# Optimization experiments

Hardware: AMD Instinct MI355X
Metric: run time of the kernel (lower is better)

Reference implementation:

```python
import jax, jax.numpy as jnp
import numpy as np

P, B, D, H, O = 512, 8, 256, 75, 128  # passage_len, batch, input_size, attn hidden, GRU hidden


def setup_inputs() -> dict:
    key = jax.random.key(0)
    ks = jax.random.split(key, 10)

    def w(k, shape, fan_in):
        return jax.random.normal(k, shape, jnp.float32) * (1.0 / np.sqrt(fan_in))

    return {
        "v": jax.random.normal(ks[0], (P, B, D), jnp.float32),
        "Wvp1": w(ks[1], (H, D), D),          # nn.Linear(input_size, hidden, bias=False)
        "Wvp2": w(ks[2], (H, D), D),
        "vw": w(ks[3], (H,), H),               # nn.Linear(hidden, 1, bias=False)
        "Wg": w(ks[4], (2 * D, 2 * D), 2 * D),  # Gate linear, no bias
        "w_ih_f": w(ks[5], (3 * O, 2 * D), 2 * D),
        "w_hh_f": w(ks[6], (3 * O, O), O),
        "b_ih_f": jnp.zeros((3 * O,), jnp.float32),
        "b_hh_f": jnp.zeros((3 * O,), jnp.float32),
        "w_ih_b": w(ks[7], (3 * O, 2 * D), 2 * D),
        "w_hh_b": w(ks[8], (3 * O, O), O),
        "b_ih_b": jnp.zeros((3 * O,), jnp.float32),
        "b_hh_b": jnp.zeros((3 * O,), jnp.float32),
    }


def _gru(x, w_ih, w_hh, b_ih, b_hh):
    # x: (T, B, in) -> hidden states (T, B, O); PyTorch GRU gate order (r, z, n)
    hdim = w_hh.shape[1]
    xp = x @ w_ih.T + b_ih  # precompute input projections: (T, B, 3O)

    def step(h, xp_t):
        gh = h @ w_hh.T + b_hh
        i_r, i_z, i_n = jnp.split(xp_t, 3, axis=-1)
        h_r, h_z, h_n = jnp.split(gh, 3, axis=-1)
        r = jax.nn.sigmoid(i_r + h_r)
        z = jax.nn.sigmoid(i_z + h_z)
        n = jnp.tanh(i_n + r * h_n)
        h_new = (1.0 - z) * n + z * h
        return h_new, h_new

    h0 = jnp.zeros((x.shape[1], hdim), x.dtype)
    _, hs = jax.lax.scan(step, h0, xp)
    return hs


def reference(v, Wvp1, Wvp2, vw, Wg,
              w_ih_f, w_hh_f, b_ih_f, b_hh_f,
              w_ih_b, w_hh_b, b_ih_b, b_hh_b):
    # dropout is inference no-op (and in the torch code its result is discarded anyway)
    Wv1 = v @ Wvp1.T  # (P, B, H) -- broadcast over key axis (dim 1 after expand)
    Wv2 = v @ Wvp2.T  # (P, B, H) -- broadcast over query axis
    # s[i, j, b, h] = tanh(Wv2[i] + Wv1[j]); softmax over i (keys)
    s = jnp.tanh(Wv2[:, None] + Wv1[None, :])          # (P, P, B, H)
    scores = jnp.einsum('ijbh,h->ijb', s, vw)          # (P, P, B)
    a = jax.nn.softmax(scores, axis=0)
    c = jnp.einsum('ijb,ibd->jbd', a, v)               # attended context (P, B, D)
    g = jnp.concatenate([v, c], axis=2)                # (P, B, 2D)
    g = jax.nn.sigmoid(g @ Wg.T) * g                   # Gate
    hf = _gru(g, w_ih_f, w_hh_f, b_ih_f, b_hh_f)
    hb = _gru(g[::-1], w_ih_b, w_hh_b, b_ih_b, b_hh_b)[::-1]
    return jnp.concatenate([hf, hb], axis=2)           # (P, B, 2O)
```

## Files before the change

kernel.cpp:

```cpp
#include <hip/hip_runtime.h>

#define TP 512
#define TB 8
#define TD 256
#define TH 75
#define THP 80
#define TO 128

#define LOG2E2 2.8853900817779268f

typedef _Float16 half_t;
typedef _Float16 half2v __attribute__((ext_vector_type(2)));
typedef _Float16 half4v __attribute__((ext_vector_type(4)));
typedef _Float16 half8v __attribute__((ext_vector_type(8)));
typedef float    float4v __attribute__((ext_vector_type(4)));

__device__ __forceinline__ float fast_rcp(float x) { return __builtin_amdgcn_rcpf(x); }
__device__ __forceinline__ float ex2(float x) {
#if __has_builtin(__builtin_amdgcn_exp2f)
    return __builtin_amdgcn_exp2f(x);
#else
    float r; asm("v_exp_f32 %0, %1" : "=v"(r) : "v"(x)); return r;
#endif
}
__device__ __forceinline__ float fast_tanh(float x) {
    return 1.0f - 2.0f * fast_rcp(1.0f + __expf(2.0f * x));
}
__device__ __forceinline__ float fast_sigmoid(float x) {
    return fast_rcp(1.0f + __expf(-x));
}
__device__ __forceinline__ float fdot2h(half2v a, half2v b, float c) {
#if __has_builtin(__builtin_amdgcn_fdot2)
    return __builtin_amdgcn_fdot2(a, b, c, false);
#else
    return c + (float)a[0] * (float)b[0] + (float)a[1] * (float)b[1];
#endif
}
#define EXT2(v, j) __builtin_shufflevector((v), (v), 2*(j), 2*(j)+1)
__device__ __forceinline__ void dot3_h8(half8v wr, half8v wz, half8v wn, half8v h,
                                        float& ar, float& az, float& an) {
    half2v h0 = EXT2(h, 0), h1 = EXT2(h, 1), h2 = EXT2(h, 2), h3 = EXT2(h, 3);
    ar = fdot2h(EXT2(wr, 0), h0, ar);
    az = fdot2h(EXT2(wz, 0), h0, az);
    an = fdot2h(EXT2(wn, 0), h0, an);
    ar = fdot2h(EXT2(wr, 1), h1, ar);
    az = fdot2h(EXT2(wz, 1), h1, az);
    an = fdot2h(EXT2(wn, 1), h1, an);
    ar = fdot2h(EXT2(wr, 2), h2, ar);
    az = fdot2h(EXT2(wz, 2), h2, az);
    an = fdot2h(EXT2(wn, 2), h2, an);
    ar = fdot2h(EXT2(wr, 3), h3, ar);
    az = fdot2h(EXT2(wz, 3), h3, az);
    an = fdot2h(EXT2(wn, 3), h3, an);
}
__device__ __forceinline__ float pair_sum_dpp(float v) {
    int i1 = __builtin_amdgcn_update_dpp(0, __builtin_bit_cast(int, v), 0xB1, 0xF, 0xF, true);
    return v + __builtin_bit_cast(float, i1);
}

__global__ __launch_bounds__(256) void prep_kernel(
    const float* __restrict__ v,
    const float* __restrict__ Wvp1, const float* __restrict__ Wvp2,
    const float* __restrict__ Wg,   const float* __restrict__ wihf,
    const float* __restrict__ wihb, const float* __restrict__ bihf,
    const float* __restrict__ bihb, const float* __restrict__ whhf,
    const float* __restrict__ whhb,
    float* __restrict__ bihC,
    half_t* __restrict__ v16, half_t* __restrict__ g16,
    half_t* __restrict__ Wg16B, half_t* __restrict__ Wih16B,
    half_t* __restrict__ whh16, half_t* __restrict__ WT16B,
    half_t* __restrict__ vT16)
{
    __shared__ half_t lt[64 * 66];

    if (blockIdx.x >= 7203) {
        int vb = blockIdx.x - 7203;
        int t = threadIdx.x;
        int b  = vb >> 5;
        int pt = (vb >> 2) & 7;
        int dt = vb & 3;
        {
            int pl = t >> 2, dseg = (t & 3) * 16;
            const float4* src = (const float4*)(v + (((pt * 64 + pl) * 8 + b) << 8) + dt * 64 + dseg);
            float4 f0 = src[0], f1 = src[1], f2 = src[2], f3 = src[3];
            half_t hv[16] = {
                (half_t)f0.x,(half_t)f0.y,(half_t)f0.z,(half_t)f0.w,
                (half_t)f1.x,(half_t)f1.y,(half_t)f1.z,(half_t)f1.w,
                (half_t)f2.x,(half_t)f2.y,(half_t)f2.z,(half_t)f2.w,
                (half_t)f3.x,(half_t)f3.y,(half_t)f3.z,(half_t)f3.w };
#pragma unroll
            for (int u = 0; u < 16; ++u) lt[(dseg + u) * 66 + pl] = hv[u];
        }
        __syncthreads();
        {
            int dl = t >> 2, pseg = (t & 3) * 16;
            half8v h0 = *(const half8v*)(lt + dl * 66 + pseg);
            half8v h1 = *(const half8v*)(lt + dl * 66 + pseg + 8);
            half8v* dst = (half8v*)(vT16 + ((b * 256 + dt * 64 + dl) << 9) + pt * 64 + pseg);
            dst[0] = h0; dst[1] = h1;
        }
        return;
    }

    int idx = blockIdx.x * 256 + threadIdx.x;
    if (idx < 1048576) {
        half_t val = (half_t)v[idx];
        v16[idx] = val;
        int row = idx >> 8, d = idx & 255;
        g16[row * 512 + d] = val;
        return;
    }
    idx -= 1048576;
    if (idx < 768) { bihC[idx] = (idx < 384) ? bihf[idx] : bihb[idx - 384]; return; }
    idx -= 768;
    if (idx < 262144) {
        int j = idx & 7, lane = (idx >> 3) & 63, kt = (idx >> 9) & 15, nt = idx >> 13;
        int o = nt * 16 + (lane & 15);
        int k = kt * 32 + ((lane >> 4) << 3) + j;
        Wg16B[idx] = (half_t)Wg[o * 512 + k];
        return;
    }
    idx -= 262144;
    if (idx < 393216) {
        int j = idx & 7, lane = (idx >> 3) & 63, kt = (idx >> 9) & 15, nt = idx >> 13;
        int o = nt * 16 + (lane & 15);
        int k = kt * 32 + ((lane >> 4) << 3) + j;
        Wih16B[idx] = (half_t)((o < 384) ? wihf[o * 512 + k] : wihb[(o - 384) * 512 + k]);
        return;
    }
    idx -= 393216;
    if (idx < 98304) {
        int d = idx / 49152, i = idx - d * 49152;
        whh16[idx] = (half_t)(d ? whhb[i] : whhf[i]);
        return;
    }
    idx -= 98304;
    if (idx < 40960) {
        int j = idx & 7, lane = (idx >> 3) & 63, kt = (idx >> 9) & 7, nt = idx >> 12;
        int o = nt * 16 + (lane & 15);
        int k = kt * 32 + ((lane >> 4) << 3) + j;
        float vv = 0.0f;
        if (o < 75)       vv = Wvp1[o * 256 + k];
        else if (o < 150) vv = Wvp2[(o - 75) * 256 + k];
        WT16B[idx] = (half_t)vv;
    }
}

__global__ __launch_bounds__(128) void wv12_kernel(
    const half_t* __restrict__ v16, const half_t* __restrict__ WT16B,
    float* __restrict__ Wv1, float* __restrict__ Wv2T)
{
    int tid = threadIdx.x;
    int lane = tid & 63, w = tid >> 6;
    int l15 = lane & 15, quad = lane >> 4;
    int r0 = blockIdx.x * 16;

    float4v acc[5];
#pragma unroll
    for (int n5 = 0; n5 < 5; ++n5) acc[n5] = (float4v){0.f, 0.f, 0.f, 0.f};

#pragma unroll
    for (int kt = 0; kt < 8; ++kt) {
        half8v a = *(const half8v*)(v16 + (r0 + l15) * 256 + kt * 32 + quad * 8);
#pragma unroll
        for (int n5 = 0; n5 < 5; ++n5) {
            int nt = w * 5 + n5;
            half8v b = *(const half8v*)(WT16B + ((nt * 8 + kt) * 64 + lane) * 8);
            acc[n5] = __builtin_amdgcn_mfma_f32_16x16x32_f16(a, b, acc[n5], 0, 0, 0);
        }
    }
#pragma unroll
    for (int n5 = 0; n5 < 5; ++n5) {
        int col = (w * 5 + n5) * 16 + l15;
#pragma unroll
        for (int r = 0; r < 4; ++r) {
            int row = r0 + quad * 4 + r;
            int p = row >> 3, b = row & 7;
            int ob = (b * TP + p) * THP;
            float val2 = LOG2E2 * acc[n5][r];
            if (col < 75)       Wv1[ob + col] = val2;
            else if (col < 80)  { Wv1[ob + col] = 0.0f;
                                  Wv2T[(b * THP + col - 75) * TP + p] = val2; }
            else if (col < 150) Wv2T[(b * THP + col - 75) * TP + p] = val2;
            else if (col < 155) Wv2T[(b * THP + col - 75) * TP + p] = 0.0f;
        }
    }
}

__global__ __launch_bounds__(256) void score_kernel(
    const float* __restrict__ Wv1, const float* __restrict__ Wv2T,
    const float* __restrict__ vw, const half_t* __restrict__ vT16,
    half_t* __restrict__ g16)
{
    int tid = threadIdx.x;
    int b  = blockIdx.x >> 6;
    int j0 = (blockIdx.x & 63) * 8;
    __shared__ float wv1j[8 * THP];
    __shared__ float vws[THP];
    __shared__ float sc[8 * TP];
    __shared__ __align__(16) half_t aL[16 * 528];

    int lane = tid & 63, w = tid >> 6;
    int l15 = lane & 15, quad = lane >> 4;

    for (int e = tid; e < 8 * 528; e += 256) aL[8 * 528 + e] = (half_t)0.0f;

    if (tid < THP) vws[tid] = (tid < TH) ? vw[tid] : 0.0f;
    for (int e = tid; e < 8 * THP; e += 256) {
        int jj = e / THP, k = e - jj * THP;
        wv1j[e] = Wv1[(b * TP + j0 + jj) * THP + k];
    }
    __syncthreads();

    float Csum = 0.0f;
    {
        const float4* c4 = (const float4*)vws;
        for (int kk = 0; kk < 20; ++kk) { float4 c = c4[kk]; Csum += c.x + c.y + c.z + c.w; }
    }

    int i0 = tid, i1 = tid + 256;
    float acc0[8] = {0.f,0.f,0.f,0.f,0.f,0.f,0.f,0.f};
    float acc1[8] = {0.f,0.f,0.f,0.f,0.f,0.f,0.f,0.f};
    const float* wvt = Wv2T + b * THP * TP;
#pragma unroll
    for (int kt = 0; kt < 5; ++kt) {
        float r0v[16], r1v[16];
#pragma unroll
        for (int u = 0; u < 16; ++u) {
            const float* colp = wvt + (kt * 16 + u) * TP;
            r0v[u] = colp[i0];
            r1v[u] = colp[i1];
        }
        const float* cp = vws + kt * 16;
#pragma unroll
        for (int jj = 0; jj < 8; ++jj) {
            const float* w1 = wv1j + jj * THP + kt * 16;
            float s0 = 0.f, s1 = 0.f;
#pragma unroll
            for (int u = 0; u < 16; ++u) {
                float cu = cp[u], wu = w1[u];
                s0 += cu * fast_rcp(1.0f + ex2(r0v[u] + wu));
                s1 += cu * fast_rcp(1.0f + ex2(r1v[u] + wu));
            }
            acc0[jj] += s0; acc1[jj] += s1;
        }
    }
#pragma unroll
    for (int jj = 0; jj < 8; ++jj) {
        sc[jj * TP + i0] = Csum - 2.0f * acc0[jj];
        sc[jj * TP + i1] = Csum - 2.0f * acc1[jj];
    }
    __syncthreads();

#pragma unroll
    for (int ps = 0; ps < 2; ++ps) {
        int jj = (tid >> 6) + ps * 4, l = tid & 63;
        float m = -1e30f;
#pragma unroll
        for (int q = 0; q < 8; ++q) m = fmaxf(m, sc[jj * TP + l + q * 64]);
#pragma unroll
        for (int s = 32; s > 0; s >>= 1) m = fmaxf(m, __shfl_xor(m, s));
        float e[8];
        float sum = 0.0f;
#pragma unroll
        for (int q = 0; q < 8; ++q) { e[q] = __expf(sc[jj * TP + l + q * 64] - m); sum += e[q]; }
#pragma unroll
        for (int s = 32; s > 0; s >>= 1) sum += __shfl_xor(sum, s);
        float inv = fast_rcp(sum);
#pragma unroll
        for (int q = 0; q < 8; ++q) aL[jj * 528 + l + q * 64] = (half_t)(e[q] * inv);
    }
    __syncthreads();

    {
        const half_t* vbase = vT16 + ((b * 256) << 9);
        float4v acc[4];
#pragma unroll
        for (int nti = 0; nti < 4; ++nti) acc[nti] = (float4v){0.f, 0.f, 0.f, 0.f};

#pragma unroll 4
        for (int kt = 0; kt < 16; ++kt) {
            half8v a = *(const half8v*)(aL + l15 * 528 + kt * 32 + quad * 8);
#pragma unroll
            for (int nti = 0; nti < 4; ++nti) {
                int d = (w * 4 + nti) * 16 + l15;
                half8v bb = *(const half8v*)(vbase + (d << 9) + kt * 32 + quad * 8);
                acc[nti] = __builtin_amdgcn_mfma_f32_16x16x32_f16(a, bb, acc[nti], 0, 0, 0);
            }
        }
        int jl0 = quad * 4;
        if (jl0 < 8) {
#pragma unroll
            for (int nti = 0; nti < 4; ++nti) {
                int d = (w * 4 + nti) * 16 + l15;
#pragma unroll
                for (int r = 0; r < 4; ++r) {
                    int j = j0 + jl0 + r;
                    g16[(j * TB + b) * 512 + 256 + d] = (half_t)acc[nti][r];
                }
            }
        }
    }
}

__global__ __launch_bounds__(256, 1) void gatexp_kernel(
    const half_t* __restrict__ g16, const half_t* __restrict__ Wg16B,
    const half_t* __restrict__ Wih16B, const float* __restrict__ bihC,
    float* __restrict__ xpf, float* __restrict__ xpb)
{
    __shared__ half_t gA[32 * 520];
    int tid = threadIdx.x;
    int r0 = blockIdx.x * 32;
    int lane = tid & 63, w = tid >> 6;
    int l15 = lane & 15, quad = lane >> 4;

    for (int e = tid; e < 2048; e += 256) {
        int row = e >> 6, c8 = e & 63;
        *(half8v*)(gA + row * 520 + c8 * 8) =
            *(const half8v*)(g16 + (r0 + row) * 512 + c8 * 8);
    }
    __syncthreads();

    float4v acc[2][8];
#pragma unroll
    for (int mi = 0; mi < 2; ++mi)
#pragma unroll
        for (int nti = 0; nti < 8; ++nti) acc[mi][nti] = (float4v){0.f, 0.f, 0.f, 0.f};

    for (int kt = 0; kt < 16; ++kt) {
        half8v a0 = *(const half8v*)(gA + l15 * 520 + kt * 32 + quad * 8);
        half8v a1 = *(const half8v*)(gA + (16 + l15) * 520 + kt * 32 + quad * 8);
#pragma unroll
        for (int nti = 0; nti < 8; ++nti) {
            half8v bb = *(const half8v*)(Wg16B + (((w * 8 + nti) * 16 + kt) * 64 + lane) * 8);
            acc[0][nti] = __builtin_amdgcn_mfma_f32_16x16x32_f16(a0, bb, acc[0][nti], 0, 0, 0);
            acc[1][nti] = __builtin_amdgcn_mfma_f32_16x16x32_f16(a1, bb, acc[1][nti], 0, 0, 0);
        }
    }
#pragma unroll
    for (int mi = 0; mi < 2; ++mi)
#pragma unroll
        for (int nti = 0; nti < 8; ++nti) {
            int colg = (w * 8 + nti) * 16 + l15;
#pragma unroll
            for (int r = 0; r < 4; ++r) {
                float gv = (float)gA[(mi * 16 + quad * 4 + r) * 520 + colg];
                acc[mi][nti][r] = fast_sigmoid(acc[mi][nti][r]) * gv;
            }
        }
    __syncthreads();
#pragma unroll
    for (int mi = 0; mi < 2; ++mi)
#pragma unroll
        for (int nti = 0; nti < 8; ++nti) {
            int colg = (w * 8 + nti) * 16 + l15;
#pragma unroll
            for (int r = 0; r < 4; ++r)
                gA[(mi * 16 + quad * 4 + r) * 520 + colg] = (half_t)acc[mi][nti][r];
        }
    __syncthreads();

    float4v c2[2][12];
#pragma unroll
    for (int mi = 0; mi < 2; ++mi)
#pragma unroll
        for (int nt2 = 0; nt2 < 12; ++nt2) {
            float bv = bihC[(w * 12 + nt2) * 16 + l15];
            c2[mi][nt2] = (float4v){bv, bv, bv, bv};
        }

    for (int kt = 0; kt < 16; ++kt) {
        half8v a0 = *(const half8v*)(gA + l15 * 520 + kt * 32 + quad * 8);
        half8v a1 = *(const half8v*)(gA + (16 + l15) * 520 + kt * 32 + quad * 8);
#pragma unroll
        for (int nt2 = 0; nt2 < 12; ++nt2) {
            half8v bb = *(const half8v*)(Wih16B + (((w * 12 + nt2) * 16 + kt) * 64 + lane) * 8);
            c2[0][nt2] = __builtin_amdgcn_mfma_f32_16x16x32_f16(a0, bb, c2[0][nt2], 0, 0, 0);
            c2[1][nt2] = __builtin_amdgcn_mfma_f32_16x16x32_f16(a1, bb, c2[1][nt2], 0, 0, 0);
        }
    }
#pragma unroll
    for (int mi = 0; mi < 2; ++mi)
#pragma unroll
        for (int nt2 = 0; nt2 < 12; ++nt2) {
            int col = (w * 12 + nt2) * 16 + l15;
            float* dst = (col < 384) ? (xpf + col) : (xpb + col - 384);
#pragma unroll
            for (int r = 0; r < 4; ++r)
                dst[(r0 + mi * 16 + quad * 4 + r) * 384] = c2[mi][nt2][r];
        }
}

__global__ __launch_bounds__(256, 1) void gru_kernel(
    const float* __restrict__ xpf, const float* __restrict__ xpb,
    const half_t* __restrict__ whh16,
    const float* __restrict__ bhhf, const float* __restrict__ bhhb,
    float* __restrict__ out)
{
    int tid = threadIdx.x;
    int dir = blockIdx.x >> 3;
    int b   = blockIdx.x & 7;
    const float* xp  = dir ? xpb  : xpf;
    const float* bhh = dir ? bhhb : bhhf;
    const half_t* wbase = whh16 + dir * 3 * TO * TO;

    __shared__ __align__(16) half_t hb[2][TO];

    int o = tid >> 1, hf = tid & 1;

    half8v wr[8], wz[8], wn[8];
    {
        const half_t* pr = wbase + (o)          * TO + hf * 64;
        const half_t* pz = wbase + (TO + o)     * TO + hf * 64;
        const half_t* pn = wbase + (2 * TO + o) * TO + hf * 64;
        asm volatile(
            "global_load_dwordx4 %0,  %24, off\n\t"
            "global_load_dwordx4 %1,  %24, off offset:16\n\t"
            "global_load_dwordx4 %2,  %24, off offset:32\n\t"
            "global_load_dwordx4 %3,  %24, off offset:48\n\t"
            "global_load_dwordx4 %4,  %24, off offset:64\n\t"
            "global_load_dwordx4 %5,  %24, off offset:80\n\t"
            "global_load_dwordx4 %6,  %24, off offset:96\n\t"
            "global_load_dwordx4 %7,  %24, off offset:112\n\t"
            "global_load_dwordx4 %8,  %25, off\n\t"
            "global_load_dwordx4 %9,  %25, off offset:16\n\t"
            "global_load_dwordx4 %10, %25, off offset:32\n\t"
            "global_load_dwordx4 %11, %25, off offset:48\n\t"
            "global_load_dwordx4 %12, %25, off offset:64\n\t"
            "global_load_dwordx4 %13, %25, off offset:80\n\t"
            "global_load_dwordx4 %14, %25, off offset:96\n\t"
            "global_load_dwordx4 %15, %25, off offset:112\n\t"
            "global_load_dwordx4 %16, %26, off\n\t"
            "global_load_dwordx4 %17, %26, off offset:16\n\t"
            "global_load_dwordx4 %18, %26, off offset:32\n\t"
            "global_load_dwordx4 %19, %26, off offset:48\n\t"
            "global_load_dwordx4 %20, %26, off offset:64\n\t"
            "global_load_dwordx4 %21, %26, off offset:80\n\t"
            "global_load_dwordx4 %22, %26, off offset:96\n\t"
            "global_load_dwordx4 %23, %26, off offset:112\n\t"
            "s_waitcnt vmcnt(0)"
            : "=&v"(wr[0]), "=&v"(wr[1]), "=&v"(wr[2]), "=&v"(wr[3]),
              "=&v"(wr[4]), "=&v"(wr[5]), "=&v"(wr[6]), "=&v"(wr[7]),
              "=&v"(wz[0]), "=&v"(wz[1]), "=&v"(wz[2]), "=&v"(wz[3]),
              "=&v"(wz[4]), "=&v"(wz[5]), "=&v"(wz[6]), "=&v"(wz[7]),
              "=&v"(wn[0]), "=&v"(wn[1]), "=&v"(wn[2]), "=&v"(wn[3]),
              "=&v"(wn[4]), "=&v"(wn[5]), "=&v"(wn[6]), "=&v"(wn[7])
            : "v"(pr), "v"(pz), "v"(pn));
    }

    float br = 0.f, bz = 0.f, bn = 0.f, h = 0.f;
    if (hf == 0) {
        br = bhh[o]; bz = bhh[TO + o]; bn = bhh[2 * TO + o];
    }
    if (tid < TO) hb[0][tid] = (half_t)0.0f;
    __syncthreads();

    float xrv[8], xzv[8], xnv[8], hist[8];

    for (int S = 0; S < TP; S += 8) {
        if (hf == 0) {
#pragma unroll
            for (int u = 0; u < 8; ++u) {
                int s = S + u;
                int tn = dir ? (TP - 1 - s) : s;
                const float* xpt = xp + (tn * TB + b) * 384;
                xrv[u] = xpt[o]; xzv[u] = xpt[TO + o]; xnv[u] = xpt[2 * TO + o];
            }
        }
#pragma unroll
        for (int u = 0; u < 8; ++u) {
            int s = S + u;
            int cur = s & 1;
            const half8v* h8 = (const half8v*)(&hb[cur][hf * 64]);
            half8v hv0 = h8[0], hv1 = h8[1], hv2 = h8[2], hv3 = h8[3];
            half8v hv4 = h8[4], hv5 = h8[5], hv6 = h8[6], hv7 = h8[7];

            float ar = 0.f, az = 0.f, an = 0.f;
            dot3_h8(wr[0], wz[0], wn[0], hv0, ar, az, an);
            dot3_h8(wr[1], wz[1], wn[1], hv1, ar, az, an);
            dot3_h8(wr[2], wz[2], wn[2], hv2, ar, az, an);
            dot3_h8(wr[3], wz[3], wn[3], hv3, ar, az, an);
            dot3_h8(wr[4], wz[4], wn[4], hv4, ar, az, an);
            dot3_h8(wr[5], wz[5], wn[5], hv5, ar, az, an);
            dot3_h8(wr[6], wz[6], wn[6], hv6, ar, az, an);
            dot3_h8(wr[7], wz[7], wn[7], hv7, ar, az, an);

            ar = pair_sum_dpp(ar);
            az = pair_sum_dpp(az);
            an = pair_sum_dpp(an);
            if (hf == 0) {
                float r = fast_sigmoid(xrv[u] + ar + br);
                float z = fast_sigmoid(xzv[u] + az + bz);
                float n = fast_tanh(xnv[u] + r * (an + bn));
                h = (1.0f - z) * n + z * h;
                hb[cur ^ 1][o] = (half_t)h;
                hist[u] = h;
            }
            asm volatile("s_waitcnt lgkmcnt(0)" ::: "memory");
            __builtin_amdgcn_s_barrier();
        }
        if (hf == 0) {
#pragma unroll
            for (int u = 0; u < 8; ++u) {
                int s = S + u;
                int t = dir ? (TP - 1 - s) : s;
                out[(t * TB + b) * 256 + dir * TO + o] = hist[u];
            }
        }
    }
}

extern "C" void kernel_launch(void* const* d_in, const int* in_sizes, int n_in,
                              void* d_out, int out_size, void* d_ws, size_t ws_size,
                              hipStream_t stream) {
    const float* v    = (const float*)d_in[0];
    const float* Wvp1 = (const float*)d_in[1];
    const float* Wvp2 = (const float*)d_in[2];
    const float* vw   = (const float*)d_in[3];
    const float* Wg   = (const float*)d_in[4];
    const float* wihf = (const float*)d_in[5];
    const float* whhf = (const float*)d_in[6];
    const float* bihf = (const float*)d_in[7];
    const float* bhhf = (const float*)d_in[8];
    const float* wihb = (const float*)d_in[9];
    const float* whhb = (const float*)d_in[10];
    const float* bihb = (const float*)d_in[11];
    const float* bhhb = (const float*)d_in[12];

    float* ws   = (float*)d_ws;
    float* bihC = ws;
    float* Wv1  = bihC + 768;
    float* Wv2T = Wv1 + 327680;
    float* xpf  = Wv2T + 327680;
    float* xpb  = xpf + 1572864;
    half_t* g16    = (half_t*)(xpb + 1572864);
    half_t* Wg16B  = g16 + 2097152;
    half_t* Wih16B = Wg16B + 262144;
    half_t* whh16  = Wih16B + 393216;
    half_t* v16    = whh16 + 98304;
    half_t* WT16B  = v16 + 1048576;
    half_t* vT16   = WT16B + 40960;
    float* out  = (float*)d_out;

    prep_kernel<<<7459, 256, 0, stream>>>(v, Wvp1, Wvp2, Wg, wihf, wihb, bihf, bihb,
                                          whhf, whhb, bihC, v16, g16,
                                          Wg16B, Wih16B, whh16, WT16B, vT16);
    wv12_kernel<<<256, 128, 0, stream>>>(v16, WT16B, Wv1, Wv2T);
    score_kernel<<<512, 256, 0, stream>>>(Wv1, Wv2T, vw, vT16, g16);
    gatexp_kernel<<<128, 256, 0, stream>>>(g16, Wg16B, Wih16B, bihC, xpf, xpb);
    gru_kernel<<<16, 256, 0, stream>>>(xpf, xpb, whh16, bhhf, bhhb, out);
}
```

Measured before the change: 417.0 us.

## Fuse score, gate projection and GRU into one flag-synchronized persistent kernel

Merges the score/attention, gate+input-projection and GRU kernels into a single launch. Block ranges take different roles and coordinate through global atomic flags with acquire/release, so GRU blocks can begin stepping once the input projections for their timesteps are ready instead of waiting for the whole previous kernel. The prep kernel is also vectorized to convert 8 elements per thread and to zero the flag array. The risks are deadlock if producer blocks are not co-resident with spinning consumers, added polling overhead, and higher register and LDS pressure from the shared fused kernel.

```diff
diff --git a/kernel.cpp b/kernel.cpp
--- a/kernel.cpp
+++ b/kernel.cpp
@@ -8,6 +8,11 @@
 #define TO 128
 
 #define LOG2E2 2.8853900817779268f
+
+#define FLAG_SCNT 0
+#define FLAG_DONE 4096
+#define FLAG_GF   4608
+#define FLAG_TOTAL 12800
 
 typedef _Float16 half_t;
 typedef _Float16 half2v __attribute__((ext_vector_type(2)));
@@ -57,6 +62,10 @@
     int i1 = __builtin_amdgcn_update_dpp(0, __builtin_bit_cast(int, v), 0xB1, 0xF, 0xF, true);
     return v + __builtin_bit_cast(float, i1);
 }
+__device__ __forceinline__ half8v cvt8(float4 f0, float4 f1) {
+    return (half8v){(half_t)f0.x,(half_t)f0.y,(half_t)f0.z,(half_t)f0.w,
+                    (half_t)f1.x,(half_t)f1.y,(half_t)f1.z,(half_t)f1.w};
+}
 
 __global__ __launch_bounds__(256) void prep_kernel(
     const float* __restrict__ v,
@@ -69,12 +78,12 @@
     half_t* __restrict__ v16, half_t* __restrict__ g16,
     half_t* __restrict__ Wg16B, half_t* __restrict__ Wih16B,
     half_t* __restrict__ whh16, half_t* __restrict__ WT16B,
-    half_t* __restrict__ vT16)
+    half_t* __restrict__ vT16, unsigned* __restrict__ flags)
 {
     __shared__ half_t lt[64 * 66];
 
-    if (blockIdx.x >= 7203) {
-        int vb = blockIdx.x - 7203;
+    if (blockIdx.x >= 907) {
+        int vb = blockIdx.x - 907;
         int t = threadIdx.x;
         int b  = vb >> 5;
         int pt = (vb >> 2) & 7;
@@ -102,47 +111,78 @@
         return;
     }
 
-    int idx = blockIdx.x * 256 + threadIdx.x;
-    if (idx < 1048576) {
-        half_t val = (half_t)v[idx];
-        v16[idx] = val;
-        int row = idx >> 8, d = idx & 255;
-        g16[row * 512 + d] = val;
+    int t8 = blockIdx.x * 256 + threadIdx.x;
+    if (t8 < 131072) {
+        int base = t8 * 8;
+        const float4* vp = (const float4*)(v + base);
+        half8v hv = cvt8(vp[0], vp[1]);
+        *(half8v*)(v16 + base) = hv;
+        int row = base >> 8, d0 = base & 255;
+        *(half8v*)(g16 + row * 512 + d0) = hv;
         return;
     }
-    idx -= 1048576;
-    if (idx < 768) { bihC[idx] = (idx < 384) ? bihf[idx] : bihb[idx - 384]; return; }
-    idx -= 768;
-    if (idx < 262144) {
-        int j = idx & 7, lane = (idx >> 3) & 63, kt = (idx >> 9) & 15, nt = idx >> 13;
+    t8 -= 131072;
+    if (t8 < 96) {
+        int base = t8 * 8;
+#pragma unroll
+        for (int u = 0; u < 8; ++u) {
+            int id = base + u;
+            bihC[id] = (id < 384) ? bihf[id] : bihb[id - 384];
+        }
+        return;
+    }
+    t8 -= 96;
+    if (t8 < 32768) {
+        int base = t8 * 8;
+        int lane = (base >> 3) & 63, kt = (base >> 9) & 15, nt = base >> 13;
         int o = nt * 16 + (lane & 15);
-        int k = kt * 32 + ((lane >> 4) << 3) + j;
-        Wg16B[idx] = (half_t)Wg[o * 512 + k];
+        int k0 = kt * 32 + ((lane >> 4) << 3);
+        const float4* sp = (const float4*)(Wg + o * 512 + k0);
+        *(half8v*)(Wg16B + base) = cvt8(sp[0], sp[1]);
         return;
     }
-    idx -= 262144;
-    if (idx < 393216) {
-        int j = idx & 7, lane = (idx >> 3) & 63, kt = (idx >> 9) & 15, nt = idx >> 13;
+    t8 -= 32768;
+    if (t8 < 49152) {
+        int base = t8 * 8;
+        int lane = (base >> 3) & 63, kt = (base >> 9) & 15, nt = base >> 13;
         int o = nt * 16 + (lane & 15);
-        int k = kt * 32 + ((lane >> 4) << 3) + j;
-        Wih16B[idx] = (half_t)((o < 384) ? wihf[o * 512 + k] : wihb[(o - 384) * 512 + k]);
+        int k0 = kt * 32 + ((lane >> 4) << 3);
+        const float4* sp = (const float4*)(((o < 384) ? (wihf + o * 512) : (wihb + (o - 384) * 512)) + k0);
+        *(half8v*)(Wih16B + base) = cvt8(sp[0], sp[1]);
         return;
     }
-    idx -= 393216;
-    if (idx < 98304) {
-        int d = idx / 49152, i = idx - d * 49152;
-        whh16[idx] = (half_t)(d ? whhb[i] : whhf[i]);
+    t8 -= 49152;
+    if (t8 < 12288) {
+        int base = t8 * 8;
+        int d = (base >= 49152) ? 1 : 0;
+        int i0 = base - d * 49152;
+        const float4* sp = (const float4*)((d ? whhb : whhf) + i0);
+        *(half8v*)(whh16 + base) = cvt8(sp[0], sp[1]);
         return;
     }
-    idx -= 98304;
-    if (idx < 40960) {
-        int j = idx & 7, lane = (idx >> 3) & 63, kt = (idx >> 9) & 7, nt = idx >> 12;
+    t8 -= 12288;
+    if (t8 < 5120) {
+        int base = t8 * 8;
+        int lane = (base >> 3) & 63, kt = (base >> 9) & 7, nt = base >> 12;
         int o = nt * 16 + (lane & 15);
-        int k = kt * 32 + ((lane >> 4) << 3) + j;
-        float vv = 0.0f;
-        if (o < 75)       vv = Wvp1[o * 256 + k];
-        else if (o < 150) vv = Wvp2[(o - 75) * 256 + k];
-        WT16B[idx] = (half_t)vv;
+        int k0 = kt * 32 + ((lane >> 4) << 3);
+        half8v hv = (half8v){(half_t)0,(half_t)0,(half_t)0,(half_t)0,
+                             (half_t)0,(half_t)0,(half_t)0,(half_t)0};
+        if (o < 75) {
+            const float4* sp = (const float4*)(Wvp1 + o * 256 + k0);
+            hv = cvt8(sp[0], sp[1]);
+        } else if (o < 150) {
+            const float4* sp = (const float4*)(Wvp2 + (o - 75) * 256 + k0);
+            hv = cvt8(sp[0], sp[1]);
+        }
+        *(half8v*)(WT16B + base) = hv;
+        return;
+    }
+    t8 -= 5120;
+    if (t8 < 1600) {
+        int base = t8 * 8;
+#pragma unroll
+        for (int u = 0; u < 8; ++u) flags[base + u] = 0u;
     }
 }
 
@@ -187,324 +227,362 @@
     }
 }
 
-__global__ __launch_bounds__(256) void score_kernel(
+__global__ __launch_bounds__(256, 3) void tail_kernel(
     const float* __restrict__ Wv1, const float* __restrict__ Wv2T,
     const float* __restrict__ vw, const half_t* __restrict__ vT16,
-    half_t* __restrict__ g16)
+    half_t* __restrict__ g16,
+    const half_t* __restrict__ Wg16B, const half_t* __restrict__ Wih16B,
+    const float* __restrict__ bihC,
+    float* __restrict__ xpf, float* __restrict__ xpb,
+    const half_t* __restrict__ whh16,
+    const float* __restrict__ bhhf, const float* __restrict__ bhhb,
+    float* __restrict__ out, unsigned* __restrict__ flags)
 {
+    __shared__ __align__(16) unsigned char smem[36160];
     int tid = threadIdx.x;
-    int b  = blockIdx.x >> 6;
-    int j0 = (blockIdx.x & 63) * 8;
-    __shared__ float wv1j[8 * THP];
-    __shared__ float vws[THP];
-    __shared__ float sc[8 * TP];
-    __shared__ __align__(16) half_t aL[16 * 528];
-
     int lane = tid & 63, w = tid >> 6;
     int l15 = lane & 15, quad = lane >> 4;
-
-    for (int e = tid; e < 8 * 528; e += 256) aL[8 * 528 + e] = (half_t)0.0f;
-
-    if (tid < THP) vws[tid] = (tid < TH) ? vw[tid] : 0.0f;
-    for (int e = tid; e < 8 * THP; e += 256) {
-        int jj = e / THP, k = e - jj * THP;
-        wv1j[e] = Wv1[(b * TP + j0 + jj) * THP + k];
-    }
-    __syncthreads();
-
-    float Csum = 0.0f;
-    {
-        const float4* c4 = (const float4*)vws;
-        for (int kk = 0; kk < 20; ++kk) { float4 c = c4[kk]; Csum += c.x + c.y + c.z + c.w; }
-    }
-
-    int i0 = tid, i1 = tid + 256;
-    float acc0[8] = {0.f,0.f,0.f,0.f,0.f,0.f,0.f,0.f};
-    float acc1[8] = {0.f,0.f,0.f,0.f,0.f,0.f,0.f,0.f};
-    const float* wvt = Wv2T + b * THP * TP;
-#pragma unroll
-    for (int kt = 0; kt < 5; ++kt) {
-        float r0v[16], r1v[16];
-#pragma unroll
-        for (int u = 0; u < 16; ++u) {
-            const float* colp = wvt + (kt * 16 + u) * TP;
-            r0v[u] = colp[i0];
-            r1v[u] = colp[i1];
-        }
-        const float* cp = vws + kt * 16;
+    unsigned bid = blockIdx.x;
+
+    if (bid < 512) {
+        int b  = bid >> 6;
+        int j0 = (bid & 63) * 8;
+        half_t* aL  = (half_t*)smem;
+        float* wv1j = (float*)(smem + 16896);
+        float* vws  = (float*)(smem + 19456);
+        float* sc   = (float*)(smem + 19776);
+
+        for (int e = tid; e < 8 * 528; e += 256) aL[8 * 528 + e] = (half_t)0.0f;
+
+        if (tid < THP) vws[tid] = (tid < TH) ? vw[tid] : 0.0f;
+        for (int e = tid; e < 8 * THP; e += 256) {
+            int jj = e / THP, k = e - jj * THP;
+            wv1j[e] = Wv1[(b * TP + j0 + jj) * THP + k];
+        }
+        __syncthreads();
+
+        float Csum = 0.0f;
+        {
+            const float4* c4 = (const float4*)vws;
+            for (int kk = 0; kk < 20; ++kk) { float4 c = c4[kk]; Csum += c.x + c.y + c.z + c.w; }
+        }
+
+        int i0 = tid, i1 = tid + 256;
+        float acc0[8] = {0.f,0.f,0.f,0.f,0.f,0.f,0.f,0.f};
+        float acc1[8] = {0.f,0.f,0.f,0.f,0.f,0.f,0.f,0.f};
+        const float* wvt = Wv2T + b * THP * TP;
+#pragma unroll
+        for (int kt = 0; kt < 5; ++kt) {
+            float r0v[16], r1v[16];
+#pragma unroll
+            for (int u = 0; u < 16; ++u) {
+                const float* colp = wvt + (kt * 16 + u) * TP;
+                r0v[u] = colp[i0];
+                r1v[u] = colp[i1];
+            }
+            const float* cp = vws + kt * 16;
+#pragma unroll
+            for (int jj = 0; jj < 8; ++jj) {
+                const float* w1 = wv1j + jj * THP + kt * 16;
+                float s0 = 0.f, s1 = 0.f;
+#pragma unroll
+                for (int u = 0; u < 16; ++u) {
+                    float cu = cp[u], wu = w1[u];
+                    s0 += cu * fast_rcp(1.0f + ex2(r0v[u] + wu));
+                    s1 += cu * fast_rcp(1.0f + ex2(r1v[u] + wu));
+                }
+                acc0[jj] += s0; acc1[jj] += s1;
+            }
+        }
 #pragma unroll
         for (int jj = 0; jj < 8; ++jj) {
-            const float* w1 = wv1j + jj * THP + kt * 16;
-            float s0 = 0.f, s1 = 0.f;
-#pragma unroll
-            for (int u = 0; u < 16; ++u) {
-                float cu = cp[u], wu = w1[u];
-                s0 += cu * fast_rcp(1.0f + ex2(r0v[u] + wu));
-                s1 += cu * fast_rcp(1.0f + ex2(r1v[u] + wu));
-            }
-            acc0[jj] += s0; acc1[jj] += s1;
-        }
-    }
-#pragma unroll
-    for (int jj = 0; jj < 8; ++jj) {
-        sc[jj * TP + i0] = Csum - 2.0f * acc0[jj];
-        sc[jj * TP + i1] = Csum - 2.0f * acc1[jj];
-    }
-    __syncthreads();
-
-#pragma unroll
-    for (int ps = 0; ps < 2; ++ps) {
-        int jj = (tid >> 6) + ps * 4, l = tid & 63;
-        float m = -1e30f;
-#pragma unroll
-        for (int q = 0; q < 8; ++q) m = fmaxf(m, sc[jj * TP + l + q * 64]);
-#pragma unroll
-        for (int s = 32; s > 0; s >>= 1) m = fmaxf(m, __shfl_xor(m, s));
-        float e[8];
-        float sum = 0.0f;
-#pragma unroll
-        for (int q = 0; q < 8; ++q) { e[q] = __expf(sc[jj * TP + l + q * 64] - m); sum += e[q]; }
-#pragma unroll
-        for (int s = 32; s > 0; s >>= 1) sum += __shfl_xor(sum, s);
-        float inv = fast_rcp(sum);
-#pragma unroll
-        for (int q = 0; q < 8; ++q) aL[jj * 528 + l + q * 64] = (half_t)(e[q] * inv);
-    }
-    __syncthreads();
-
-    {
-        const half_t* vbase = vT16 + ((b * 256) << 9);
-        float4v acc[4];
-#pragma unroll
-        for (int nti = 0; nti < 4; ++nti) acc[nti] = (float4v){0.f, 0.f, 0.f, 0.f};
-
+            sc[jj * TP + i0] = Csum - 2.0f * acc0[jj];
+            sc[jj * TP + i1] = Csum - 2.0f * acc1[jj];
+        }
+        __syncthreads();
+
+#pragma unroll
+        for (int ps = 0; ps < 2; ++ps) {
+            int jj = (tid >> 6) + ps * 4, l = tid & 63;
+            float m = -1e30f;
+#pragma unroll
+            for (int q = 0; q < 8; ++q) m = fmaxf(m, sc[jj * TP + l + q * 64]);
+#pragma unroll
+            for (int s = 32; s > 0; s >>= 1) m = fmaxf(m, __shfl_xor(m, s));
+            float e[8];
+            float sum = 0.0f;
+#pragma unroll
+            for (int q = 0; q < 8; ++q) { e[q] = __expf(sc[jj * TP + l + q * 64] - m); sum += e[q]; }
+#pragma unroll
+            for (int s = 32; s > 0; s >>= 1) sum += __shfl_xor(sum, s);
+            float inv = fast_rcp(sum);
+#pragma unroll
+            for (int q = 0; q < 8; ++q) aL[jj * 528 + l + q * 64] = (half_t)(e[q] * inv);
+        }
+        __syncthreads();
+
+        {
+            const half_t* vbase = vT16 + ((b * 256) << 9);
+            float4v acc[4];
+#pragma unroll
+            for (int nti = 0; nti < 4; ++nti) acc[nti] = (float4v){0.f, 0.f, 0.f, 0.f};
 #pragma unroll 4
+            for (int kt = 0; kt < 16; ++kt) {
+                half8v a = *(const half8v*)(aL + l15 * 528 + kt * 32 + quad * 8);
+#pragma unroll
+                for (int nti = 0; nti < 4; ++nti) {
+                    int d = (w * 4 + nti) * 16 + l15;
+                    half8v bb = *(const half8v*)(vbase + (d << 9) + kt * 32 + quad * 8);
+                    acc[nti] = __builtin_amdgcn_mfma_f32_16x16x32_f16(a, bb, acc[nti], 0, 0, 0);
+                }
+            }
+            int jl0 = quad * 4;
+            if (jl0 < 8) {
+#pragma unroll
+                for (int nti = 0; nti < 4; ++nti) {
+                    int d = (w * 4 + nti) * 16 + l15;
+#pragma unroll
+                    for (int r = 0; r < 4; ++r) {
+                        int j = j0 + jl0 + r;
+                        g16[(j * TB + b) * 512 + 256 + d] = (half_t)acc[nti][r];
+                    }
+                }
+            }
+        }
+        __syncthreads();
+        if (tid == 0)
+            __hip_atomic_fetch_add(flags + FLAG_SCNT + (bid & 63) * 64, 1u,
+                                   __ATOMIC_RELEASE, __HIP_MEMORY_SCOPE_AGENT);
+
+    } else if (bid < 640) {
+        int gb = (int)bid - 512;
+        if (tid == 0) {
+            while (__hip_atomic_load(flags + FLAG_SCNT + (gb >> 1) * 64,
+                                     __ATOMIC_ACQUIRE, __HIP_MEMORY_SCOPE_AGENT) < 8u)
+                __builtin_amdgcn_s_sleep(16);
+        }
+        __syncthreads();
+
+        half_t* gA = (half_t*)smem;
+        int r0 = gb * 32;
+
+        for (int e = tid; e < 2048; e += 256) {
+            int row = e >> 6, c8 = e & 63;
+            *(half8v*)(gA + row * 520 + c8 * 8) =
+                *(const half8v*)(g16 + (r0 + row) * 512 + c8 * 8);
+        }
+        __syncthreads();
+
+        float4v acc[2][8];
+#pragma unroll
+        for (int mi = 0; mi < 2; ++mi)
+#pragma unroll
+            for (int nti = 0; nti < 8; ++nti) acc[mi][nti] = (float4v){0.f, 0.f, 0.f, 0.f};
+
         for (int kt = 0; kt < 16; ++kt) {
-            half8v a = *(const half8v*)(aL + l15 * 528 + kt * 32 + quad * 8);
-#pragma unroll
-            for (int nti = 0; nti < 4; ++nti) {
-                int d = (w * 4 + nti) * 16 + l15;
-                half8v bb = *(const half8v*)(vbase + (d << 9) + kt * 32 + quad * 8);
-                acc[nti] = __builtin_amdgcn_mfma_f32_16x16x32_f16(a, bb, acc[nti], 0, 0, 0);
-            }
-        }
-        int jl0 = quad * 4;
-        if (jl0 < 8) {
-#pragma unroll
-            for (int nti = 0; nti < 4; ++nti) {
-                int d = (w * 4 + nti) * 16 + l15;
+            half8v a0 = *(const half8v*)(gA + l15 * 520 + kt * 32 + quad * 8);
+            half8v a1 = *(const half8v*)(gA + (16 + l15) * 520 + kt * 32 + quad * 8);
+#pragma unroll
+            for (int nti = 0; nti < 8; ++nti) {
+                half8v bb = *(const half8v*)(Wg16B + (((w * 8 + nti) * 16 + kt) * 64 + lane) * 8);
+                acc[0][nti] = __builtin_amdgcn_mfma_f32_16x16x32_f16(a0, bb, acc[0][nti], 0, 0, 0);
+                acc[1][nti] = __builtin_amdgcn_mfma_f32_16x16x32_f16(a1, bb, acc[1][nti], 0, 0, 0);
+            }
+        }
+#pragma unroll
+        for (int mi = 0; mi < 2; ++mi)
+#pragma unroll
+            for (int nti = 0; nti < 8; ++nti) {
+                int colg = (w * 8 + nti) * 16 + l15;
 #pragma unroll
                 for (int r = 0; r < 4; ++r) {
-                    int j = j0 + jl0 + r;
-                    g16[(j * TB + b) * 512 + 256 + d] = (half_t)acc[nti][r];
-                }
-            }
-        }
-    }
-}
-
-__global__ __launch_bounds__(256, 1) void gatexp_kernel(
-    const half_t* __restrict__ g16, const half_t* __restrict__ Wg16B,
-    const half_t* __restrict__ Wih16B, const float* __restrict__ bihC,
-    float* __restrict__ xpf, float* __restrict__ xpb)
-{
-    __shared__ half_t gA[32 * 520];
-    int tid = threadIdx.x;
-    int r0 = blockIdx.x * 32;
-    int lane = tid & 63, w = tid >> 6;
-    int l15 = lane & 15, quad = lane >> 4;
-
-    for (int e = tid; e < 2048; e += 256) {
-        int row = e >> 6, c8 = e & 63;
-        *(half8v*)(gA + row * 520 + c8 * 8) =
-            *(const half8v*)(g16 + (r0 + row) * 512 + c8 * 8);
-    }
-    __syncthreads();
-
-    float4v acc[2][8];
-#pragma unroll
-    for (int mi = 0; mi < 2; ++mi)
-#pragma unroll
-        for (int nti = 0; nti < 8; ++nti) acc[mi][nti] = (float4v){0.f, 0.f, 0.f, 0.f};
-
-    for (int kt = 0; kt < 16; ++kt) {
-        half8v a0 = *(const half8v*)(gA + l15 * 520 + kt * 32 + quad * 8);
-        half8v a1 = *(const half8v*)(gA + (16 + l15) * 520 + kt * 32 + quad * 8);
-#pragma unroll
-        for (int nti = 0; nti < 8; ++nti) {
-            half8v bb = *(const half8v*)(Wg16B + (((w * 8 + nti) * 16 + kt) * 64 + lane) * 8);
-            acc[0][nti] = __builtin_amdgcn_mfma_f32_16x16x32_f16(a0, bb, acc[0][nti], 0, 0, 0);
-            acc[1][nti] = __builtin_amdgcn_mfma_f32_16x16x32_f16(a1, bb, acc[1][nti], 0, 0, 0);
-        }
-    }
-#pragma unroll
-    for (int mi = 0; mi < 2; ++mi)
-#pragma unroll
-        for (int nti = 0; nti < 8; ++nti) {
-            int colg = (w * 8 + nti) * 16 + l15;
-#pragma unroll
-            for (int r = 0; r < 4; ++r) {
-                float gv = (float)gA[(mi * 16 + quad * 4 + r) * 520 + colg];
-                acc[mi][nti][r] = fast_sigmoid(acc[mi][nti][r]) * gv;
-            }
-        }
-    __syncthreads();
-#pragma unroll
-    for (int mi = 0; mi < 2; ++mi)
-#pragma unroll
-        for (int nti = 0; nti < 8; ++nti) {
-            int colg = (w * 8 + nti) * 16 + l15;
-#pragma unroll
-            for (int r = 0; r < 4; ++r)
-                gA[(mi * 16 + quad * 4 + r) * 520 + colg] = (half_t)acc[mi][nti][r];
-        }
-    __syncthreads();
-
-    float4v c2[2][12];
-#pragma unroll
-    for (int mi = 0; mi < 2; ++mi)
-#pragma unroll
-        for (int nt2 = 0; nt2 < 12; ++nt2) {
-            float bv = bihC[(w * 12 + nt2) * 16 + l15];
-            c2[mi][nt2] = (float4v){bv, bv, bv, bv};
-        }
-
-    for (int kt = 0; kt < 16; ++kt) {
-        half8v a0 = *(const half8v*)(gA + l15 * 520 + kt * 32 + quad * 8);
-        half8v a1 = *(const half8v*)(gA + (16 + l15) * 520 + kt * 32 + quad * 8);
-#pragma unroll
-        for (int nt2 = 0; nt2 < 12; ++nt2) {
-            half8v bb = *(const half8v*)(Wih16B + (((w * 12 + nt2) * 16 + kt) * 64 + lane) * 8);
-            c2[0][nt2] = __builtin_amdgcn_mfma_f32_16x16x32_f16(a0, bb, c2[0][nt2], 0, 0, 0);
-            c2[1][nt2] = __builtin_amdgcn_mfma_f32_16x16x32_f16(a1, bb, c2[1][nt2], 0, 0, 0);
-        }
-    }
-#pragma unroll
-    for (int mi = 0; mi < 2; ++mi)
-#pragma unroll
-        for (int nt2 = 0; nt2 < 12; ++nt2) {
-            int col = (w * 12 + nt2) * 16 + l15;
-            float* dst = (col < 384) ? (xpf + col) : (xpb + col - 384);
-#pragma unroll
-            for (int r = 0; r < 4; ++r)
-                dst[(r0 + mi * 16 + quad * 4 + r) * 384] = c2[mi][nt2][r];
-        }
-}
-
-__global__ __launch_bounds__(256, 1) void gru_kernel(
-    const float* __restrict__ xpf, const float* __restrict__ xpb,
-    const half_t* __restrict__ whh16,
-    const float* __restrict__ bhhf, const float* __restrict__ bhhb,
-    float* __restrict__ out)
-{
-    int tid = threadIdx.x;
-    int dir = blockIdx.x >> 3;
-    int b   = blockIdx.x & 7;
-    const float* xp  = dir ? xpb  : xpf;
-    const float* bhh = dir ? bhhb : bhhf;
-    const half_t* wbase = whh16 + dir * 3 * TO * TO;
-
-    __shared__ __align__(16) half_t hb[2][TO];
-
-    int o = tid >> 1, hf = tid & 1;
-
-    half8v wr[8], wz[8], wn[8];
-    {
-        const half_t* pr = wbase + (o)          * TO + hf * 64;
-        const half_t* pz = wbase + (TO + o)     * TO + hf * 64;
-        const half_t* pn = wbase + (2 * TO + o) * TO + hf * 64;
-        asm volatile(
-            "global_load_dwordx4 %0,  %24, off\n\t"
-            "global_load_dwordx4 %1,  %24, off offset:16\n\t"
-            "global_load_dwordx4 %2,  %24, off offset:32\n\t"
-            "global_load_dwordx4 %3,  %24, off offset:48\n\t"
-            "global_load_dwordx4 %4,  %24, off offset:64\n\t"
-            "global_load_dwordx4 %5,  %24, off offset:80\n\t"
-            "global_load_dwordx4 %6,  %24, off offset:96\n\t"
-            "global_load_dwordx4 %7,  %24, off offset:112\n\t"
-            "global_load_dwordx4 %8,  %25, off\n\t"
-            "global_load_dwordx4 %9,  %25, off offset:16\n\t"
-            "global_load_dwordx4 %10, %25, off offset:32\n\t"
-            "global_load_dwordx4 %11, %25, off offset:48\n\t"
-            "global_load_dwordx4 %12, %25, off offset:64\n\t"
-            "global_load_dwordx4 %13, %25, off offset:80\n\t"
-            "global_load_dwordx4 %14, %25, off offset:96\n\t"
-            "global_load_dwordx4 %15, %25, off offset:112\n\t"
-            "global_load_dwordx4 %16, %26, off\n\t"
-            "global_load_dwordx4 %17, %26, off offset:16\n\t"
-            "global_load_dwordx4 %18, %26, off offset:32\n\t"
-            "global_load_dwordx4 %19, %26, off offset:48\n\t"
-            "global_load_dwordx4 %20, %26, off offset:64\n\t"
-            "global_load_dwordx4 %21, %26, off offset:80\n\t"
-            "global_load_dwordx4 %22, %26, off offset:96\n\t"
-            "global_load_dwordx4 %23, %26, off offset:112\n\t"
-            "s_waitcnt vmcnt(0)"
-            : "=&v"(wr[0]), "=&v"(wr[1]), "=&v"(wr[2]), "=&v"(wr[3]),
-              "=&v"(wr[4]), "=&v"(wr[5]), "=&v"(wr[6]), "=&v"(wr[7]),
-              "=&v"(wz[0]), "=&v"(wz[1]), "=&v"(wz[2]), "=&v"(wz[3]),
-              "=&v"(wz[4]), "=&v"(wz[5]), "=&v"(wz[6]), "=&v"(wz[7]),
-              "=&v"(wn[0]), "=&v"(wn[1]), "=&v"(wn[2]), "=&v"(wn[3]),
-              "=&v"(wn[4]), "=&v"(wn[5]), "=&v"(wn[6]), "=&v"(wn[7])
-            : "v"(pr), "v"(pz), "v"(pn));
-    }
-
-    float br = 0.f, bz = 0.f, bn = 0.f, h = 0.f;
-    if (hf == 0) {
-        br = bhh[o]; bz = bhh[TO + o]; bn = bhh[2 * TO + o];
-    }
-    if (tid < TO) hb[0][tid] = (half_t)0.0f;
-    __syncthreads();
-
-    float xrv[8], xzv[8], xnv[8], hist[8];
-
-    for (int S = 0; S < TP; S += 8) {
+                    float gv = (float)gA[(mi * 16 + quad * 4 + r) * 520 + colg];
+                    acc[mi][nti][r] = fast_sigmoid(acc[mi][nti][r]) * gv;
+                }
+            }
+        __syncthreads();
+#pragma unroll
+        for (int mi = 0; mi < 2; ++mi)
+#pragma unroll
+            for (int nti = 0; nti < 8; ++nti) {
+                int colg = (w * 8 + nti) * 16 + l15;
+#pragma unroll
+                for (int r = 0; r < 4; ++r)
+                    gA[(mi * 16 + quad * 4 + r) * 520 + colg] = (half_t)acc[mi][nti][r];
+            }
+        __syncthreads();
+
+        float4v c2[2][12];
+#pragma unroll
+        for (int mi = 0; mi < 2; ++mi)
+#pragma unroll
+            for (int nt2 = 0; nt2 < 12; ++nt2) {
+                float bv = bihC[(w * 12 + nt2) * 16 + l15];
+                c2[mi][nt2] = (float4v){bv, bv, bv, bv};
+            }
+
+        for (int kt = 0; kt < 16; ++kt) {
+            half8v a0 = *(const half8v*)(gA + l15 * 520 + kt * 32 + quad * 8);
+            half8v a1 = *(const half8v*)(gA + (16 + l15) * 520 + kt * 32 + quad * 8);
+#pragma unroll
+            for (int nt2 = 0; nt2 < 12; ++nt2) {
+                half8v bb = *(const half8v*)(Wih16B + (((w * 12 + nt2) * 16 + kt) * 64 + lane) * 8);
+                c2[0][nt2] = __builtin_amdgcn_mfma_f32_16x16x32_f16(a0, bb, c2[0][nt2], 0, 0, 0);
+                c2[1][nt2] = __builtin_amdgcn_mfma_f32_16x16x32_f16(a1, bb, c2[1][nt2], 0, 0, 0);
+            }
+        }
+#pragma unroll
+        for (int mi = 0; mi < 2; ++mi)
+#pragma unroll
+            for (int nt2 = 0; nt2 < 12; ++nt2) {
+                int col = (w * 12 + nt2) * 16 + l15;
+                float* dst = (col < 384) ? (xpf + col) : (xpb + col - 384);
+#pragma unroll
+                for (int r = 0; r < 4; ++r)
+                    dst[(r0 + mi * 16 + quad * 4 + r) * 384] = c2[mi][nt2][r];
+            }
+        __syncthreads();
+        if (tid == 0) {
+            __hip_atomic_store(flags + FLAG_GF + gb * 64, 1u,
+                               __ATOMIC_RELEASE, __HIP_MEMORY_SCOPE_AGENT);
+            __hip_atomic_fetch_add(flags + FLAG_DONE + (gb & 7) * 64, 1u,
+                                   __ATOMIC_RELEASE, __HIP_MEMORY_SCOPE_AGENT);
+        }
+
+    } else {
+        int ci  = (int)bid - 640;
+        int dir = ci >> 3;
+        int b   = ci & 7;
+        const float* xp  = dir ? xpb  : xpf;
+        const float* bhh = dir ? bhhb : bhhf;
+        const half_t* wbase = whh16 + dir * 3 * TO * TO;
+
+        half_t (*hb)[TO] = (half_t (*)[TO])smem;
+        int* gsh = (int*)(smem + 512);
+
+        int o = tid >> 1, hf = tid & 1;
+
+        half8v wr[8], wz[8], wn[8];
+        {
+            const half_t* pr = wbase + (o)          * TO + hf * 64;
+            const half_t* pz = wbase + (TO + o)     * TO + hf * 64;
+            const half_t* pn = wbase + (2 * TO + o) * TO + hf * 64;
+            asm volatile(
+                "global_load_dwordx4 %0,  %24, off\n\t"
+                "global_load_dwordx4 %1,  %24, off offset:16\n\t"
+                "global_load_dwordx4 %2,  %24, off offset:32\n\t"
+                "global_load_dwordx4 %3,  %24, off offset:48\n\t"
+                "global_load_dwordx4 %4,  %24, off offset:64\n\t"
+                "global_load_dwordx4 %5,  %24, off offset:80\n\t"
+                "global_load_dwordx4 %6,  %24, off offset:96\n\t"
+                "global_load_dwordx4 %7,  %24, off offset:112\n\t"
+                "global_load_dwordx4 %8,  %25, off\n\t"
+                "global_load_dwordx4 %9,  %25, off offset:16\n\t"
+                "global_load_dwordx4 %10, %25, off offset:32\n\t"
+                "global_load_dwordx4 %11, %25, off offset:48\n\t"
+                "global_load_dwordx4 %12, %25, off offset:64\n\t"
+                "global_load_dwordx4 %13, %25, off offset:80\n\t"
+                "global_load_dwordx4 %14, %25, off offset:96\n\t"
+                "global_load_dwordx4 %15, %25, off offset:112\n\t"
+                "global_load_dwordx4 %16, %26, off\n\t"
+                "global_load_dwordx4 %17, %26, off offset:16\n\t"
+                "global_load_dwordx4 %18, %26, off offset:32\n\t"
+                "global_load_dwordx4 %19, %26, off offset:48\n\t"
+                "global_load_dwordx4 %20, %26, off offset:64\n\t"
+                "global_load_dwordx4 %21, %26, off offset:80\n\t"
+                "global_load_dwordx4 %22, %26, off offset:96\n\t"
+                "global_load_dwordx4 %23, %26, off offset:112\n\t"
+                "s_waitcnt vmcnt(0)"
+                : "=&v"(wr[0]), "=&v"(wr[1]), "=&v"(wr[2]), "=&v"(wr[3]),
+                  "=&v"(wr[4]), "=&v"(wr[5]), "=&v"(wr[6]), "=&v"(wr[7]),
+                  "=&v"(wz[0]), "=&v"(wz[1]), "=&v"(wz[2]), "=&v"(wz[3]),
+                  "=&v"(wz[4]), "=&v"(wz[5]), "=&v"(wz[6]), "=&v"(wz[7]),
+                  "=&v"(wn[0]), "=&v"(wn[1]), "=&v"(wn[2]), "=&v"(wn[3]),
+                  "=&v"(wn[4]), "=&v"(wn[5]), "=&v"(wn[6]), "=&v"(wn[7])
+                : "v"(pr), "v"(pz), "v"(pn));
+        }
+
+        float br = 0.f, bz = 0.f, bn = 0.f, h = 0.f;
         if (hf == 0) {
+            br = bhh[o]; bz = bhh[TO + o]; bn = bhh[2 * TO + o];
+        }
+        if (tid < TO) hb[0][tid] = (half_t)0.0f;
+        if (tid == 0) *gsh = 0;
+        __syncthreads();
+
+        float xrv[8], xzv[8], xnv[8], hist[8];
+        bool alldone = false;
+
+        for (int S = 0; S < TP; S += 8) {
+            if (!alldone) {
+                if (tid == 0) {
+                    int tnlo = dir ? (TP - 8 - S) : S;
+                    int gb0 = tnlo >> 2, gb1 = (tnlo + 7) >> 2;
+                    for (;;) {
+                        unsigned sum = 0;
+#pragma unroll
+                        for (int q = 0; q < 8; ++q)
+                            sum += __hip_atomic_load(flags + FLAG_DONE + q * 64,
+                                                     __ATOMIC_ACQUIRE, __HIP_MEMORY_SCOPE_AGENT);
+                        if (sum == 128u) { *gsh = 1; break; }
+                        if (__hip_atomic_load(flags + FLAG_GF + gb0 * 64,
+                                              __ATOMIC_ACQUIRE, __HIP_MEMORY_SCOPE_AGENT) &&
+                            __hip_atomic_load(flags + FLAG_GF + gb1 * 64,
+                                              __ATOMIC_ACQUIRE, __HIP_MEMORY_SCOPE_AGENT)) break;
+                        __builtin_amdgcn_s_sleep(16);
+                    }
+                }
+                __syncthreads();
+                alldone = (*gsh != 0);
+            }
+            if (hf == 0) {
+#pragma unroll
+                for (int u = 0; u < 8; ++u) {
+                    int s = S + u;
+                    int tn = dir ? (TP - 1 - s) : s;
+                    const float* xpt = xp + (tn * TB + b) * 384;
+                    xrv[u] = xpt[o]; xzv[u] = xpt[TO + o]; xnv[u] = xpt[2 * TO + o];
+                }
+            }
 #pragma unroll
             for (int u = 0; u < 8; ++u) {
                 int s = S + u;
-                int tn = dir ? (TP - 1 - s) : s;
-                const float* xpt = xp + (tn * TB + b) * 384;
-                xrv[u] = xpt[o]; xzv[u] = xpt[TO + o]; xnv[u] = xpt[2 * TO + o];
-            }
-        }
-#pragma unroll
-        for (int u = 0; u < 8; ++u) {
-            int s = S + u;
-            int cur = s & 1;
-            const half8v* h8 = (const half8v*)(&hb[cur][hf * 64]);
-            half8v hv0 = h8[0], hv1 = h8[1], hv2 = h8[2], hv3 = h8[3];
-            half8v hv4 = h8[4], hv5 = h8[5], hv6 = h8[6], hv7 = h8[7];
-
-            float ar = 0.f, az = 0.f, an = 0.f;
-            dot3_h8(wr[0], wz[0], wn[0], hv0, ar, az, an);
-            dot3_h8(wr[1], wz[1], wn[1], hv1, ar, az, an);
-            dot3_h8(wr[2], wz[2], wn[2], hv2, ar, az, an);
-            dot3_h8(wr[3], wz[3], wn[3], hv3, ar, az, an);
-            dot3_h8(wr[4], wz[4], wn[4], hv4, ar, az, an);
-            dot3_h8(wr[5], wz[5], wn[5], hv5, ar, az, an);
-            dot3_h8(wr[6], wz[6], wn[6], hv6, ar, az, an);
-            dot3_h8(wr[7], wz[7], wn[7], hv7, ar, az, an);
-
-            ar = pair_sum_dpp(ar);
-            az = pair_sum_dpp(az);
-            an = pair_sum_dpp(an);
+                int cur = s & 1;
+                const half8v* h8 = (const half8v*)(&hb[cur][hf * 64]);
+                half8v hv0 = h8[0], hv1 = h8[1], hv2 = h8[2], hv3 = h8[3];
+                half8v hv4 = h8[4], hv5 = h8[5], hv6 = h8[6], hv7 = h8[7];
+
+                float ar = 0.f, az = 0.f, an = 0.f;
+                dot3_h8(wr[0], wz[0], wn[0], hv0, ar, az, an);
+                dot3_h8(wr[1], wz[1], wn[1], hv1, ar, az, an);
+                dot3_h8(wr[2], wz[2], wn[2], hv2, ar, az, an);
+                dot3_h8(wr[3], wz[3], wn[3], hv3, ar, az, an);
+                dot3_h8(wr[4], wz[4], wn[4], hv4, ar, az, an);
+                dot3_h8(wr[5], wz[5], wn[5], hv5, ar, az, an);
+                dot3_h8(wr[6], wz[6], wn[6], hv6, ar, az, an);
+                dot3_h8(wr[7], wz[7], wn[7], hv7, ar, az, an);
+
+                ar = pair_sum_dpp(ar);
+                az = pair_sum_dpp(az);
+                an = pair_sum_dpp(an);
+                if (hf == 0) {
+                    float r = fast_sigmoid(xrv[u] + ar + br);
+                    float z = fast_sigmoid(xzv[u] + az + bz);
+                    float n = fast_tanh(xnv[u] + r * (an + bn));
+                    h = (1.0f - z) * n + z * h;
+                    hb[cur ^ 1][o] = (half_t)h;
+                    hist[u] = h;
+                }
+                asm volatile("s_waitcnt lgkmcnt(0)" ::: "memory");
+                __builtin_amdgcn_s_barrier();
+            }
             if (hf == 0) {
-                float r = fast_sigmoid(xrv[u] + ar + br);
-                float z = fast_sigmoid(xzv[u] + az + bz);
-                float n = fast_tanh(xnv[u] + r * (an + bn));
-                h = (1.0f - z) * n + z * h;
-                hb[cur ^ 1][o] = (half_t)h;
-                hist[u] = h;
-            }
-            asm volatile("s_waitcnt lgkmcnt(0)" ::: "memory");
-            __builtin_amdgcn_s_barrier();
-        }
-        if (hf == 0) {
-#pragma unroll
-            for (int u = 0; u < 8; ++u) {
-                int s = S + u;
-                int t = dir ? (TP - 1 - s) : s;
-                out[(t * TB + b) * 256 + dir * TO + o] = hist[u];
+#pragma unroll
+                for (int u = 0; u < 8; ++u) {
+                    int s = S + u;
+                    int t = dir ? (TP - 1 - s) : s;
+                    out[(t * TB + b) * 256 + dir * TO + o] = hist[u];
+                }
             }
         }
     }
@@ -540,13 +618,14 @@
     half_t* v16    = whh16 + 98304;
     half_t* WT16B  = v16 + 1048576;
     half_t* vT16   = WT16B + 40960;
+    unsigned* flags = (unsigned*)(vT16 + 1048576);
     float* out  = (float*)d_out;
 
-    prep_kernel<<<7459, 256, 0, stream>>>(v, Wvp1, Wvp2, Wg, wihf, wihb, bihf, bihb,
+    prep_kernel<<<1163, 256, 0, stream>>>(v, Wvp1, Wvp2, Wg, wihf, wihb, bihf, bihb,
                                           whhf, whhb, bihC, v16, g16,
-                                          Wg16B, Wih16B, whh16, WT16B, vT16);
+                                          Wg16B, Wih16B, whh16, WT16B, vT16, flags);
     wv12_kernel<<<256, 128, 0, stream>>>(v16, WT16B, Wv1, Wv2T);
-    score_kernel<<<512, 256, 0, stream>>>(Wv1, Wv2T, vw, vT16, g16);
-    gatexp_kernel<<<128, 256, 0, stream>>>(g16, Wg16B, Wih16B, bihC, xpf, xpb);
-    gru_kernel<<<16, 256, 0, stream>>>(xpf, xpb, whh16, bhhf, bhhb, out);
-}
+    tail_kernel<<<656, 256, 0, stream>>>(Wv1, Wv2T, vw, vT16, g16,
+                                         Wg16B, Wih16B, bihC, xpf, xpb,
+                                         whh16, bhhf, bhhb, out, flags);
+}
```

New measurement: 555.9 us. +33.3%, slower.
